# Kernel optimization log

Measured on AMD Instinct MI355X. Metric: run time of the kernel, lower is better.

The kernel has to match this reference:

```python
import jax, jax.numpy as jnp
import numpy as np

N_EMBD = 384
N_HEAD = 6
HEAD_SIZE = N_EMBD // N_HEAD
D_FF = 4 * N_EMBD
LN_EPS = 1e-3  # keras LayerNormalization default epsilon


def setup_inputs() -> dict:
    key = jax.random.key(0)
    ks = jax.random.split(key, 12)
    B, T = 4, 2048
    s = 1.0 / np.sqrt(N_EMBD)
    return {
        "x": jax.random.normal(ks[0], (B, T, N_EMBD), dtype=jnp.float32),
        "Wq": jax.random.normal(ks[1], (N_EMBD, N_EMBD), dtype=jnp.float32) * s,
        "Wk": jax.random.normal(ks[2], (N_EMBD, N_EMBD), dtype=jnp.float32) * s,
        "Wv": jax.random.normal(ks[3], (N_EMBD, N_EMBD), dtype=jnp.float32) * s,
        "Wo": jax.random.normal(ks[4], (N_EMBD, N_EMBD), dtype=jnp.float32) * s,
        "bo": jnp.zeros((N_EMBD,), dtype=jnp.float32),
        "W1": jax.random.normal(ks[5], (N_EMBD, D_FF), dtype=jnp.float32) * s,
        "b1": jnp.zeros((D_FF,), dtype=jnp.float32),
        "W2": jax.random.normal(ks[6], (D_FF, N_EMBD), dtype=jnp.float32) * (1.0 / np.sqrt(D_FF)),
        "b2": jnp.zeros((N_EMBD,), dtype=jnp.float32),
        "g1": jnp.ones((N_EMBD,), dtype=jnp.float32),
        "be1": jnp.zeros((N_EMBD,), dtype=jnp.float32),
        "g2": jnp.ones((N_EMBD,), dtype=jnp.float32),
        "be2": jnp.zeros((N_EMBD,), dtype=jnp.float32),
    }


def _layer_norm(x, gamma, beta):
    mu = jnp.mean(x, axis=-1, keepdims=True)
    var = jnp.mean(jnp.square(x - mu), axis=-1, keepdims=True)
    return (x - mu) * jax.lax.rsqrt(var + LN_EPS) * gamma + beta


def _block(x, Wq, Wk, Wv, Wo, bo, W1, b1, W2, b2, g1, be1, g2, be2):
    B, T, C = x.shape
    H, D = N_HEAD, HEAD_SIZE
    q = (x @ Wq).reshape(B, T, H, D).transpose(0, 2, 1, 3)  # [B,H,T,D]
    k = (x @ Wk).reshape(B, T, H, D).transpose(0, 2, 1, 3)
    v = (x @ Wv).reshape(B, T, H, D).transpose(0, 2, 1, 3)
    scores = jnp.einsum("bhqd,bhkd->bhqk", q, k) / jnp.sqrt(jnp.float32(D))
    causal = jnp.tril(jnp.ones((T, T), dtype=bool))
    scores = jnp.where(causal, scores, jnp.float32(-1e9))
    attn = jax.nn.softmax(scores, axis=-1)  # dropout is identity at inference
    out = jnp.einsum("bhqk,bhkd->bhqd", attn, v)
    out = out.transpose(0, 2, 1, 3).reshape(B, T, H * D)
    y = out @ Wo + bo
    x = _layer_norm(x + y, g1, be1)
    y = jax.nn.relu(x @ W1 + b1) @ W2 + b2
    return _layer_norm(x + y, g2, be2)


def reference(x, Wq, Wk, Wv, Wo, bo, W1, b1, W2, b2, g1, be1, g2, be2):
    return _block(x, Wq, Wk, Wv, Wo, bo, W1, b1, W2, b2, g1, be1, g2, be2)
```

## Files before the change

kernel.cpp:

```cpp
#include <hip/hip_runtime.h>

#define C_DIM  384
#define HEADS  6
#define HD     64
#define FF_DIM 1536
#define LN_EPS 1e-3f
#define TSEQ   2048
#define BATCH  4
#define LOG2E  1.4426950408889634f
#define QK_SCALE 0.18033688011112042f

typedef __attribute__((ext_vector_type(4))) float          f32x4;
typedef __attribute__((ext_vector_type(4))) float          float4_t;
typedef __attribute__((ext_vector_type(8))) short          bfrag;
typedef __attribute__((ext_vector_type(4))) unsigned short ushort4_t;
typedef __attribute__((ext_vector_type(8))) unsigned short ushort8_t;

__device__ inline unsigned short f2bf(float f) {
    unsigned int u = __builtin_bit_cast(unsigned int, f);
    u += 0x7fff + ((u >> 16) & 1);
    return (unsigned short)(u >> 16);
}
__device__ inline unsigned short f2bf_t(float f) {
    return (unsigned short)(__builtin_bit_cast(unsigned int, f) >> 16);
}

__device__ inline void gload_lds16(const void* g, void* l) {
    __builtin_amdgcn_global_load_lds(
        (const __attribute__((address_space(1))) unsigned int*)g,
        (__attribute__((address_space(3))) unsigned int*)l,
        16, 0, 0);
}

__global__ __launch_bounds__(256)
void transpose_w4(const float* __restrict__ Wq, const float* __restrict__ Wk,
                  const float* __restrict__ Wv, const float* __restrict__ Wo,
                  unsigned short* __restrict__ Dq, unsigned short* __restrict__ Dk,
                  unsigned short* __restrict__ Dv, unsigned short* __restrict__ Do_)
{
    __shared__ float tile[32][33];
    const int z = blockIdx.z;
    const float* W = z == 0 ? Wq : (z == 1 ? Wk : (z == 2 ? Wv : Wo));
    unsigned short* D = z == 0 ? Dq : (z == 1 ? Dk : (z == 2 ? Dv : Do_));
    const int tx = threadIdx.x, ty = threadIdx.y;
    const int n0 = blockIdx.x * 32, k0 = blockIdx.y * 32;
    #pragma unroll
    for (int i = 0; i < 32; i += 8)
        tile[ty + i][tx] = W[(size_t)(k0 + ty + i) * C_DIM + n0 + tx];
    __syncthreads();
    #pragma unroll
    for (int i = 0; i < 32; i += 8)
        D[(size_t)(n0 + ty + i) * C_DIM + k0 + tx] = f2bf(tile[tx][ty + i]);
}

__global__ __launch_bounds__(256)
void transpose_w(const float* __restrict__ W, unsigned short* __restrict__ Wt, int K, int N)
{
    __shared__ float tile[32][33];
    const int tx = threadIdx.x, ty = threadIdx.y;
    const int n0 = blockIdx.x * 32, k0 = blockIdx.y * 32;
    #pragma unroll
    for (int i = 0; i < 32; i += 8)
        tile[ty + i][tx] = W[(size_t)(k0 + ty + i) * N + n0 + tx];
    __syncthreads();
    #pragma unroll
    for (int i = 0; i < 32; i += 8)
        Wt[(size_t)(n0 + ty + i) * K + k0 + tx] = f2bf(tile[tx][ty + i]);
}

__global__ __launch_bounds__(256)
void cvt_f32_bf16_x4(const float* __restrict__ in, unsigned short* __restrict__ out, int n4)
{
    int i = blockIdx.x * 256 + threadIdx.x;
    if (i >= n4) return;
    float4_t v = ((const float4_t*)in)[i];
    ushort4_t o = { f2bf(v.x), f2bf(v.y), f2bf(v.z), f2bf(v.w) };
    ((ushort4_t*)out)[i] = o;
}

__global__ __launch_bounds__(256)
void vtrans_kernel(const unsigned short* __restrict__ qkv,
                   unsigned short* __restrict__ vt,
                   unsigned short* __restrict__ ktc)
{
    __shared__ unsigned short tile[32][34];
    const int tx = threadIdx.x, ty = threadIdx.y;
    const int bh = blockIdx.z, b = bh / HEADS, h = bh % HEADS;
    const int t0 = blockIdx.x * 32, d0 = blockIdx.y * 32;
    #pragma unroll
    for (int i = 0; i < 32; i += 8) {
        tile[ty + i][tx] = qkv[(size_t)(b * TSEQ + t0 + ty + i) * 1152 + 2 * C_DIM + h * HD + d0 + tx];
        ktc[((size_t)bh * TSEQ + t0 + ty + i) * HD + d0 + tx] =
            qkv[(size_t)(b * TSEQ + t0 + ty + i) * 1152 + C_DIM + h * HD + d0 + tx];
    }
    __syncthreads();
    #pragma unroll
    for (int i = 0; i < 32; i += 8)
        vt[((size_t)bh * HD + d0 + ty + i) * TSEQ + t0 + tx] = tile[tx][ty + i];
}

template<int OBF16, int BIAS, int RELU, int QSCALE>
__global__ __launch_bounds__(256)
void gemm_lds(const unsigned short* __restrict__ A, const unsigned short* __restrict__ Bt,
              const float* __restrict__ bias, void* __restrict__ Cv,
              int M, int N, int K)
{
    __shared__ __align__(16) unsigned short As[16 * 512];
    __shared__ __align__(16) unsigned short Bs[16 * 512];

    const int t = threadIdx.x, lane = t & 63, w = t >> 6;
    const int ln16 = lane & 15, hi16 = lane >> 4;
    const int wr = w >> 1, wc = w & 1;
    const int row0 = blockIdx.y * 128, col0 = blockIdx.x * 128;

    f32x4 acc[4][4] = {};

    for (int k0 = 0; k0 < K; k0 += 64) {
        #pragma unroll
        for (int i = 0; i < 4; ++i) {
            const int f  = w * 4 + i;
            const int ks = f >> 3, rf = f & 7;
            const int row = rf * 16 + ln16;
            const int kc  = k0 + ks * 32 + hi16 * 8;
            gload_lds16(&A [(size_t)(row0 + row) * K + kc], &As[f * 512]);
            gload_lds16(&Bt[(size_t)(col0 + row) * K + kc], &Bs[f * 512]);
        }
        __syncthreads();
        #pragma unroll
        for (int ks = 0; ks < 2; ++ks) {
            bfrag a[4], b[4];
            #pragma unroll
            for (int i = 0; i < 4; ++i)
                a[i] = *(const bfrag*)&As[(ks * 8 + wr * 4 + i) * 512 + lane * 8];
            #pragma unroll
            for (int j = 0; j < 4; ++j)
                b[j] = *(const bfrag*)&Bs[(ks * 8 + wc * 4 + j) * 512 + lane * 8];
            #pragma unroll
            for (int i = 0; i < 4; ++i)
                #pragma unroll
                for (int j = 0; j < 4; ++j)
                    acc[i][j] = __builtin_amdgcn_mfma_f32_16x16x32_bf16(a[i], b[j], acc[i][j], 0, 0, 0);
        }
        __syncthreads();
    }

    #pragma unroll
    for (int j = 0; j < 4; ++j) {
        const int col = col0 + wc * 64 + j * 16 + ln16;
        const float bv = BIAS ? bias[col] : 0.0f;
        const float sc = (QSCALE && col < C_DIM) ? QK_SCALE : 1.0f;
        #pragma unroll
        for (int i = 0; i < 4; ++i) {
            #pragma unroll
            for (int e = 0; e < 4; ++e) {
                const int row = row0 + wr * 64 + i * 16 + hi16 * 4 + e;
                float v = acc[i][j][e] + bv;
                if (RELU) v = fmaxf(v, 0.0f);
                if (QSCALE) v *= sc;
                if (OBF16) ((unsigned short*)Cv)[(size_t)row * N + col] = f2bf(v);
                else       ((float*)Cv)[(size_t)row * N + col] = v;
            }
        }
    }
}

template<int OBF16, int BIAS, int RELU>
__global__ __launch_bounds__(256)
void gemm_lds64(const unsigned short* __restrict__ A, const unsigned short* __restrict__ Bt,
                const float* __restrict__ bias, void* __restrict__ Cv,
                int M, int N, int K)
{
    __shared__ __align__(16) unsigned short As[8 * 512];
    __shared__ __align__(16) unsigned short Bs[16 * 512];

    const int t = threadIdx.x, lane = t & 63, w = t >> 6;
    const int ln16 = lane & 15, hi16 = lane >> 4;
    const int wr = w >> 1, wc = w & 1;
    const int row0 = blockIdx.y * 64, col0 = blockIdx.x * 128;

    f32x4 acc[2][4] = {};

    for (int k0 = 0; k0 < K; k0 += 64) {
        #pragma unroll
        for (int i = 0; i < 2; ++i) {
            const int f  = w * 2 + i;
            const int ks = f >> 2, rf = f & 3;
            gload_lds16(&A[(size_t)(row0 + rf * 16 + ln16) * K + k0 + ks * 32 + hi16 * 8],
                        &As[f * 512]);
        }
        #pragma unroll
        for (int i = 0; i < 4; ++i) {
            const int f  = w * 4 + i;
            const int ks = f >> 3, cf = f & 7;
            gload_lds16(&Bt[(size_t)(col0 + cf * 16 + ln16) * K + k0 + ks * 32 + hi16 * 8],
                        &Bs[f * 512]);
        }
        __syncthreads();
        #pragma unroll
        for (int ks = 0; ks < 2; ++ks) {
            bfrag a[2], b[4];
            #pragma unroll
            for (int i = 0; i < 2; ++i)
                a[i] = *(const bfrag*)&As[(ks * 4 + wr * 2 + i) * 512 + lane * 8];
            #pragma unroll
            for (int j = 0; j < 4; ++j)
                b[j] = *(const bfrag*)&Bs[(ks * 8 + wc * 4 + j) * 512 + lane * 8];
            #pragma unroll
            for (int i = 0; i < 2; ++i)
                #pragma unroll
                for (int j = 0; j < 4; ++j)
                    acc[i][j] = __builtin_amdgcn_mfma_f32_16x16x32_bf16(a[i], b[j], acc[i][j], 0, 0, 0);
        }
        __syncthreads();
    }

    #pragma unroll
    for (int j = 0; j < 4; ++j) {
        const int col = col0 + wc * 64 + j * 16 + ln16;
        const float bv = BIAS ? bias[col] : 0.0f;
        #pragma unroll
        for (int i = 0; i < 2; ++i) {
            #pragma unroll
            for (int e = 0; e < 4; ++e) {
                const int row = row0 + wr * 32 + i * 16 + hi16 * 4 + e;
                float v = acc[i][j][e] + bv;
                if (RELU) v = fmaxf(v, 0.0f);
                if (OBF16) ((unsigned short*)Cv)[(size_t)row * N + col] = f2bf(v);
                else       ((float*)Cv)[(size_t)row * N + col] = v;
            }
        }
    }
}

__device__ inline void qk16(const bfrag (&qf)[2][2], const bfrag (&kf)[4][2],
                            f32x4 (&sf)[2][4])
{
    #pragma unroll
    for (int jt = 0; jt < 4; ++jt)
        #pragma unroll
        for (int ks = 0; ks < 2; ++ks) {
            sf[0][jt] = __builtin_amdgcn_mfma_f32_16x16x32_bf16(qf[0][ks], kf[jt][ks], sf[0][jt], 0, 0, 0);
            sf[1][jt] = __builtin_amdgcn_mfma_f32_16x16x32_bf16(qf[1][ks], kf[jt][ks], sf[1][jt], 0, 0, 0);
        }
}

__device__ inline void softmax_pv(f32x4 (&sf)[2][4], const bfrag (&vf)[4][2],
                                  f32x4 (&acc)[2][4],
                                  float (&mrow)[2][4], float (&lrow)[2][4],
                                  unsigned short (*Ps)[72],
                                  int tok0, int kt, bool last, int ln16, int hi16)
{
    float lmax[2][4];
    bool need = false;
    #pragma unroll
    for (int rf = 0; rf < 2; ++rf)
        #pragma unroll
        for (int e = 0; e < 4; ++e) {
            const int row = tok0 + rf * 16 + hi16 * 4 + e;
            float mx = -1e30f;
            #pragma unroll
            for (int jt = 0; jt < 4; ++jt) {
                float sv = sf[rf][jt][e];
                if (last && (kt * 64 + jt * 16 + ln16 > row)) sv = -1e30f;
                mx = fmaxf(mx, sv);
            }
            lmax[rf][e] = mx;
            need = need || (mx > mrow[rf][e] + 8.0f);
        }
    if (__any(need)) {
        #pragma unroll
        for (int rf = 0; rf < 2; ++rf)
            #pragma unroll
            for (int e = 0; e < 4; ++e) {
                float rm = lmax[rf][e];
                rm = fmaxf(rm, __shfl_xor(rm, 1));
                rm = fmaxf(rm, __shfl_xor(rm, 2));
                rm = fmaxf(rm, __shfl_xor(rm, 4));
                rm = fmaxf(rm, __shfl_xor(rm, 8));
                const float mn = fmaxf(mrow[rf][e], rm);
                const float corr = exp2f(mrow[rf][e] - mn);
                mrow[rf][e] = mn;
                lrow[rf][e] *= corr;
                #pragma unroll
                for (int dt = 0; dt < 4; ++dt) acc[rf][dt][e] *= corr;
            }
    }

    #pragma unroll
    for (int rf = 0; rf < 2; ++rf)
        #pragma unroll
        for (int jt = 0; jt < 4; ++jt)
            #pragma unroll
            for (int e = 0; e < 4; ++e) {
                const int row = tok0 + rf * 16 + hi16 * 4 + e;
                float sv = sf[rf][jt][e];
                if (last && (kt * 64 + jt * 16 + ln16 > row)) sv = -1e30f;
                const float pe = exp2f(sv - mrow[rf][e]);
                lrow[rf][e] += pe;
                Ps[rf * 16 + hi16 * 4 + e][jt * 16 + ln16] = f2bf_t(pe);
            }

    bfrag pf[2][2];
    #pragma unroll
    for (int rf = 0; rf < 2; ++rf)
        #pragma unroll
        for (int ks = 0; ks < 2; ++ks)
            pf[rf][ks] = *(const bfrag*)&Ps[rf * 16 + ln16][ks * 32 + hi16 * 8];
    #pragma unroll
    for (int ks = 0; ks < 2; ++ks)
        #pragma unroll
        for (int rf = 0; rf < 2; ++rf)
            #pragma unroll
            for (int dt = 0; dt < 4; ++dt)
                acc[rf][dt] = __builtin_amdgcn_mfma_f32_16x16x32_bf16(pf[rf][ks], vf[dt][ks], acc[rf][dt], 0, 0, 0);
}

__global__ __launch_bounds__(64)
void attn_kernel(const unsigned short* __restrict__ qkv,
                 const unsigned short* __restrict__ ktc,
                 const unsigned short* __restrict__ vt,
                 unsigned short* __restrict__ att,
                 unsigned short* __restrict__ pacc,
                 float* __restrict__ pml)
{
    __shared__ __align__(16) unsigned short Ps[32][72];
    const int lane = threadIdx.x;
    const int ln16 = lane & 15, hi16 = lane >> 4;
    const int bid = blockIdx.x;
    const int xcd = bid & 7;
    const int i   = bid >> 3;
    int bh, qw, kt0, kte, ck = 0;
    bool heavy;
    if (i < 192) {
        qw = 63 - (i / 6);
        const int r = i % 6;
        bh = xcd * 3 + (r >> 1);
        ck = r & 1;
        const int NT = (qw >> 1) + 1;
        const int half = NT >> 1;
        kt0 = ck ? half : 0;
        kte = ck ? NT : half;
        heavy = true;
    } else {
        const int j = i - 192;
        qw = 31 - (j / 3);
        bh = xcd * 3 + (j % 3);
        kt0 = 0;
        kte = (qw >> 1) + 1;
        heavy = false;
    }
    const int NTfull = (qw >> 1) + 1;
    const int b = bh / HEADS, h = bh % HEADS;
    const int tok0 = qw * 32;
    const size_t qrow0 = (size_t)b * TSEQ;

    bfrag qf[2][2];
    #pragma unroll
    for (int rf = 0; rf < 2; ++rf)
        #pragma unroll
        for (int ks = 0; ks < 2; ++ks)
            qf[rf][ks] = *(const bfrag*)&qkv[(qrow0 + tok0 + rf * 16 + ln16) * 1152 + h * HD + ks * 32 + hi16 * 8];

    f32x4 acc[2][4] = {};
    float mrow[2][4], lrow[2][4];
    #pragma unroll
    for (int rf = 0; rf < 2; ++rf)
        #pragma unroll
        for (int e = 0; e < 4; ++e) { mrow[rf][e] = -1e30f; lrow[rf][e] = 0.0f; }

    const unsigned short* Kb = ktc + (size_t)bh * TSEQ * HD;
    const unsigned short* Vb = vt  + (size_t)bh * HD * TSEQ;

    bfrag kf[4][2];
    #pragma unroll
    for (int jt = 0; jt < 4; ++jt)
        #pragma unroll
        for (int ks = 0; ks < 2; ++ks)
            kf[jt][ks] = *(const bfrag*)&Kb[(size_t)(kt0 * 64 + jt * 16 + ln16) * HD + ks * 32 + hi16 * 8];

    for (int kt = kt0; kt < kte; ++kt) {
        bfrag vf[4][2];
        #pragma unroll
        for (int dt = 0; dt < 4; ++dt)
            #pragma unroll
            for (int ks = 0; ks < 2; ++ks)
                vf[dt][ks] = *(const bfrag*)&Vb[(size_t)(dt * 16 + ln16) * TSEQ + kt * 64 + ks * 32 + hi16 * 8];

        f32x4 sf[2][4] = {};
        qk16(qf, kf, sf);

        if (kt + 1 < kte) {
            #pragma unroll
            for (int jt = 0; jt < 4; ++jt)
                #pragma unroll
                for (int ks = 0; ks < 2; ++ks)
                    kf[jt][ks] = *(const bfrag*)&Kb[(size_t)((kt + 1) * 64 + jt * 16 + ln16) * HD + ks * 32 + hi16 * 8];
        }

        softmax_pv(sf, vf, acc, mrow, lrow, Ps, tok0, kt, kt == NTfull - 1, ln16, hi16);
    }

    float lsum[2][4];
    #pragma unroll
    for (int rf = 0; rf < 2; ++rf)
        #pragma unroll
        for (int e = 0; e < 4; ++e) {
            float l = lrow[rf][e];
            l += __shfl_xor(l, 1);
            l += __shfl_xor(l, 2);
            l += __shfl_xor(l, 4);
            l += __shfl_xor(l, 8);
            lsum[rf][e] = l;
        }

    if (!heavy) {
        #pragma unroll
        for (int rf = 0; rf < 2; ++rf)
            #pragma unroll
            for (int e = 0; e < 4; ++e) {
                const float inv = 1.0f / lsum[rf][e];
                const size_t row = qrow0 + tok0 + rf * 16 + hi16 * 4 + e;
                #pragma unroll
                for (int dt = 0; dt < 4; ++dt)
                    att[row * C_DIM + h * HD + dt * 16 + ln16] = f2bf(acc[rf][dt][e] * inv);
            }
    } else {
        const int sidx = bh * 32 + (qw - 32);
        const size_t pb = (size_t)sidx * 2 + ck;
        #pragma unroll
        for (int rf = 0; rf < 2; ++rf)
            #pragma unroll
            for (int dt = 0; dt < 4; ++dt)
                #pragma unroll
                for (int e = 0; e < 4; ++e) {
                    const int row = rf * 16 + hi16 * 4 + e;
                    pacc[(pb * 32 + row) * 64 + dt * 16 + ln16] = f2bf(acc[rf][dt][e]);
                }
        if (ln16 == 0) {
            #pragma unroll
            for (int rf = 0; rf < 2; ++rf)
                #pragma unroll
                for (int e = 0; e < 4; ++e) {
                    const int row = rf * 16 + hi16 * 4 + e;
                    pml[pb * 64 + row * 2 + 0] = mrow[rf][e];
                    pml[pb * 64 + row * 2 + 1] = lsum[rf][e];
                }
        }
    }
}

__global__ __launch_bounds__(256)
void attn_combine(const unsigned short* __restrict__ pacc,
                  const float* __restrict__ pml,
                  unsigned short* __restrict__ att)
{
    const int sidx = blockIdx.x;
    const int bh = sidx >> 5;
    const int qw = 32 + (sidx & 31);
    const int b = bh / HEADS, h = bh % HEADS;
    const int tid = threadIdx.x;
    const int row = tid >> 3;
    const int d0  = (tid & 7) * 8;

    const float m0 = pml[((size_t)sidx * 2 + 0) * 64 + row * 2 + 0];
    const float l0 = pml[((size_t)sidx * 2 + 0) * 64 + row * 2 + 1];
    const float m1 = pml[((size_t)sidx * 2 + 1) * 64 + row * 2 + 0];
    const float l1 = pml[((size_t)sidx * 2 + 1) * 64 + row * 2 + 1];
    const float M  = fmaxf(m0, m1);
    const float w0 = exp2f(m0 - M), w1 = exp2f(m1 - M);
    const float invL = 1.0f / (l0 * w0 + l1 * w1);

    ushort8_t a0 = *(const ushort8_t*)&pacc[(((size_t)sidx * 2 + 0) * 32 + row) * 64 + d0];
    ushort8_t a1 = *(const ushort8_t*)&pacc[(((size_t)sidx * 2 + 1) * 32 + row) * 64 + d0];
    ushort8_t rv;
    #pragma unroll
    for (int k = 0; k < 8; ++k) {
        const float v0 = __builtin_bit_cast(float, (unsigned int)a0[k] << 16);
        const float v1 = __builtin_bit_cast(float, (unsigned int)a1[k] << 16);
        rv[k] = f2bf((v0 * w0 + v1 * w1) * invL);
    }
    const size_t grow = (size_t)b * TSEQ + qw * 32 + row;
    *(ushort8_t*)&att[grow * C_DIM + h * HD + d0] = rv;
}

template<int WB>
__global__ __launch_bounds__(256)
void ln_residual_kernel(const float* __restrict__ A, const float* __restrict__ R,
                        const float* __restrict__ gamma, const float* __restrict__ beta,
                        float* __restrict__ out, unsigned short* __restrict__ outb, int Mrows)
{
    const int lane = threadIdx.x & 63;
    const int wv   = threadIdx.x >> 6;
    const int row  = blockIdx.x * 4 + wv;
    if (row >= Mrows) return;
    const size_t off = (size_t)row * C_DIM;

    float v[6];
    float sum = 0.0f;
    #pragma unroll
    for (int j = 0; j < 6; ++j) {
        const int c = lane + 64 * j;
        v[j] = A[off + c] + R[off + c];
        sum += v[j];
    }
    #pragma unroll
    for (int o = 1; o < 64; o <<= 1) sum += __shfl_xor(sum, o);
    const float mu = sum * (1.0f / C_DIM);

    float sq = 0.0f;
    #pragma unroll
    for (int j = 0; j < 6; ++j) { const float d = v[j] - mu; sq = fmaf(d, d, sq); }
    #pragma unroll
    for (int o = 1; o < 64; o <<= 1) sq += __shfl_xor(sq, o);
    const float rstd = rsqrtf(sq * (1.0f / C_DIM) + LN_EPS);

    #pragma unroll
    for (int j = 0; j < 6; ++j) {
        const int c = lane + 64 * j;
        const float r = (v[j] - mu) * rstd * gamma[c] + beta[c];
        out[off + c] = r;
        if (WB) outb[off + c] = f2bf(r);
    }
}

extern "C" void kernel_launch(void* const* d_in, const int* in_sizes, int n_in,
                              void* d_out, int out_size, void* d_ws, size_t ws_size,
                              hipStream_t stream)
{
    const float* x   = (const float*)d_in[0];
    const float* Wq  = (const float*)d_in[1];
    const float* Wk  = (const float*)d_in[2];
    const float* Wv  = (const float*)d_in[3];
    const float* Wo  = (const float*)d_in[4];
    const float* bo  = (const float*)d_in[5];
    const float* W1  = (const float*)d_in[6];
    const float* b1  = (const float*)d_in[7];
    const float* W2  = (const float*)d_in[8];
    const float* b2  = (const float*)d_in[9];
    const float* g1  = (const float*)d_in[10];
    const float* be1 = (const float*)d_in[11];
    const float* g2  = (const float*)d_in[12];
    const float* be2 = (const float*)d_in[13];
    float* out = (float*)d_out;

    const int M = BATCH * TSEQ;
    const size_t MC = (size_t)M * C_DIM;

    char* ws = (char*)d_ws;
    unsigned short* qkv = (unsigned short*)ws;
    unsigned short* vt  = (unsigned short*)(ws + (size_t)M*1152*2);
    unsigned short* att = (unsigned short*)(ws + (size_t)M*1152*2 + (size_t)BATCH*HEADS*HD*TSEQ*2);
    unsigned short* h1  = (unsigned short*)ws;
    char* p2 = ws + (size_t)M*1152*2 + (size_t)BATCH*HEADS*HD*TSEQ*2 + MC*2;
    unsigned short* xb  = (unsigned short*)p2;
    unsigned short* ktc = xb;
    float* y   = (float*)(p2 + MC*2);
    float* x1  = (float*)(p2 + MC*2 + MC*4);
    unsigned short* x1b = (unsigned short*)(p2 + MC*2 + 2*MC*4);
    char* p3 = p2 + MC*2 + 2*MC*4 + MC*2;
    unsigned short* Wqkv_t = (unsigned short*)p3;
    unsigned short* Wo_t   = Wqkv_t + (size_t)3*C_DIM*C_DIM;
    unsigned short* W1_t   = Wo_t   + (size_t)C_DIM*C_DIM;
    unsigned short* W2_t   = W1_t   + (size_t)FF_DIM*C_DIM;

    unsigned short* pacc = (unsigned short*)(p2 + MC*2);
    float* pml = (float*)(p2 + MC*2 + (size_t)1536*32*64*2);

    dim3 b256(256), b328(32, 8);

    transpose_w4<<<dim3(C_DIM/32, C_DIM/32, 4), b328, 0, stream>>>(
        Wq, Wk, Wv, Wo,
        Wqkv_t, Wqkv_t + (size_t)C_DIM*C_DIM, Wqkv_t + (size_t)2*C_DIM*C_DIM, Wo_t);
    transpose_w<<<dim3(FF_DIM/32, C_DIM/32), b328, 0, stream>>>(W1, W1_t, C_DIM, FF_DIM);
    transpose_w<<<dim3(C_DIM/32, FF_DIM/32), b328, 0, stream>>>(W2, W2_t, FF_DIM, C_DIM);

    cvt_f32_bf16_x4<<<dim3((MC/4 + 255)/256), b256, 0, stream>>>(x, xb, (int)(MC/4));

    gemm_lds<1, 0, 0, 1><<<dim3(3*C_DIM/128, M/128), b256, 0, stream>>>(
        xb, Wqkv_t, nullptr, qkv, M, 3*C_DIM, C_DIM);

    vtrans_kernel<<<dim3(TSEQ/32, HD/32, BATCH*HEADS), b328, 0, stream>>>(qkv, vt, ktc);

    attn_kernel<<<dim3(2304), dim3(64), 0, stream>>>(qkv, ktc, vt, att, pacc, pml);
    attn_combine<<<dim3(768), b256, 0, stream>>>(pacc, pml, att);

    gemm_lds64<0, 1, 0><<<dim3(C_DIM/128, M/64), b256, 0, stream>>>(
        att, Wo_t, bo, y, M, C_DIM, C_DIM);

    ln_residual_kernel<1><<<dim3(M/4), b256, 0, stream>>>(x, y, g1, be1, x1, x1b, M);

    gemm_lds<1, 1, 1, 0><<<dim3(FF_DIM/128, M/128), b256, 0, stream>>>(
        x1b, W1_t, b1, h1, M, FF_DIM, C_DIM);

    gemm_lds64<0, 1, 0><<<dim3(C_DIM/128, M/64), b256, 0, stream>>>(
        h1, W2_t, b2, y, M, C_DIM, FF_DIM);

    ln_residual_kernel<0><<<dim3(M/4), b256, 0, stream>>>(x1, y, g2, be2, out, nullptr, M);
}
```

Baseline: 204.1 us.

## Merge weight transposes, fuse K relayout into QKV GEMM, drop fp32 x1

Combines the three weight transpose kernels into one launch. Moves the K-head relayout into the QKV GEMM epilogue so vtrans only transposes V. Adds s_setprio around the MFMA blocks in attention. Removes the fp32 copy of the post-LN1 activations and feeds the bf16 copy into the final residual LayerNorm, which cuts memory traffic but lowers residual precision.

```diff
diff --git a/kernel.cpp b/kernel.cpp
--- a/kernel.cpp
+++ b/kernel.cpp
@@ -24,6 +24,9 @@
 __device__ inline unsigned short f2bf_t(float f) {
     return (unsigned short)(__builtin_bit_cast(unsigned int, f) >> 16);
 }
+__device__ inline float bf2f(unsigned short u) {
+    return __builtin_bit_cast(float, (unsigned int)u << 16);
+}
 
 __device__ inline void gload_lds16(const void* g, void* l) {
     __builtin_amdgcn_global_load_lds(
@@ -33,39 +36,37 @@
 }
 
 __global__ __launch_bounds__(256)
-void transpose_w4(const float* __restrict__ Wq, const float* __restrict__ Wk,
-                  const float* __restrict__ Wv, const float* __restrict__ Wo,
-                  unsigned short* __restrict__ Dq, unsigned short* __restrict__ Dk,
-                  unsigned short* __restrict__ Dv, unsigned short* __restrict__ Do_)
+void transpose_all(const float* __restrict__ Wq, const float* __restrict__ Wk,
+                   const float* __restrict__ Wv, const float* __restrict__ Wo,
+                   const float* __restrict__ W1, const float* __restrict__ W2,
+                   unsigned short* __restrict__ Dqkv, unsigned short* __restrict__ Do_,
+                   unsigned short* __restrict__ D1, unsigned short* __restrict__ D2)
 {
     __shared__ float tile[32][33];
-    const int z = blockIdx.z;
-    const float* W = z == 0 ? Wq : (z == 1 ? Wk : (z == 2 ? Wv : Wo));
-    unsigned short* D = z == 0 ? Dq : (z == 1 ? Dk : (z == 2 ? Dv : Do_));
+    const int bidx = blockIdx.x;
+    const float* W; unsigned short* D;
+    int K, N, nx, ny;
+    if (bidx < 576) {
+        const int z = bidx / 144, r = bidx % 144;
+        W = z == 0 ? Wq : (z == 1 ? Wk : (z == 2 ? Wv : Wo));
+        D = z == 3 ? Do_ : Dqkv + (size_t)z * C_DIM * C_DIM;
+        K = N = C_DIM; nx = r % 12; ny = r / 12;
+    } else if (bidx < 1152) {
+        const int r = bidx - 576;
+        W = W1; D = D1; K = C_DIM; N = FF_DIM; nx = r % 48; ny = r / 48;
+    } else {
+        const int r = bidx - 1152;
+        W = W2; D = D2; K = FF_DIM; N = C_DIM; nx = r % 12; ny = r / 12;
+    }
     const int tx = threadIdx.x, ty = threadIdx.y;
-    const int n0 = blockIdx.x * 32, k0 = blockIdx.y * 32;
-    #pragma unroll
-    for (int i = 0; i < 32; i += 8)
-        tile[ty + i][tx] = W[(size_t)(k0 + ty + i) * C_DIM + n0 + tx];
-    __syncthreads();
-    #pragma unroll
-    for (int i = 0; i < 32; i += 8)
-        D[(size_t)(n0 + ty + i) * C_DIM + k0 + tx] = f2bf(tile[tx][ty + i]);
-}
-
-__global__ __launch_bounds__(256)
-void transpose_w(const float* __restrict__ W, unsigned short* __restrict__ Wt, int K, int N)
-{
-    __shared__ float tile[32][33];
-    const int tx = threadIdx.x, ty = threadIdx.y;
-    const int n0 = blockIdx.x * 32, k0 = blockIdx.y * 32;
+    const int n0 = nx * 32, k0 = ny * 32;
     #pragma unroll
     for (int i = 0; i < 32; i += 8)
         tile[ty + i][tx] = W[(size_t)(k0 + ty + i) * N + n0 + tx];
     __syncthreads();
     #pragma unroll
     for (int i = 0; i < 32; i += 8)
-        Wt[(size_t)(n0 + ty + i) * K + k0 + tx] = f2bf(tile[tx][ty + i]);
+        D[(size_t)(n0 + ty + i) * K + k0 + tx] = f2bf(tile[tx][ty + i]);
 }
 
 __global__ __launch_bounds__(256)
@@ -80,29 +81,26 @@
 
 __global__ __launch_bounds__(256)
 void vtrans_kernel(const unsigned short* __restrict__ qkv,
-                   unsigned short* __restrict__ vt,
-                   unsigned short* __restrict__ ktc)
+                   unsigned short* __restrict__ vt)
 {
     __shared__ unsigned short tile[32][34];
     const int tx = threadIdx.x, ty = threadIdx.y;
     const int bh = blockIdx.z, b = bh / HEADS, h = bh % HEADS;
     const int t0 = blockIdx.x * 32, d0 = blockIdx.y * 32;
     #pragma unroll
-    for (int i = 0; i < 32; i += 8) {
+    for (int i = 0; i < 32; i += 8)
         tile[ty + i][tx] = qkv[(size_t)(b * TSEQ + t0 + ty + i) * 1152 + 2 * C_DIM + h * HD + d0 + tx];
-        ktc[((size_t)bh * TSEQ + t0 + ty + i) * HD + d0 + tx] =
-            qkv[(size_t)(b * TSEQ + t0 + ty + i) * 1152 + C_DIM + h * HD + d0 + tx];
-    }
     __syncthreads();
     #pragma unroll
     for (int i = 0; i < 32; i += 8)
         vt[((size_t)bh * HD + d0 + ty + i) * TSEQ + t0 + tx] = tile[tx][ty + i];
 }
 
-template<int OBF16, int BIAS, int RELU, int QSCALE>
+template<int OBF16, int BIAS, int RELU, int QSCALE, int KSPLIT>
 __global__ __launch_bounds__(256)
 void gemm_lds(const unsigned short* __restrict__ A, const unsigned short* __restrict__ Bt,
               const float* __restrict__ bias, void* __restrict__ Cv,
+              unsigned short* __restrict__ ktc,
               int M, int N, int K)
 {
     __shared__ __align__(16) unsigned short As[16 * 512];
@@ -146,9 +144,11 @@
 
     #pragma unroll
     for (int j = 0; j < 4; ++j) {
-        const int col = col0 + wc * 64 + j * 16 + ln16;
+        const int cbase = col0 + wc * 64 + j * 16;
+        const int col = cbase + ln16;
         const float bv = BIAS ? bias[col] : 0.0f;
         const float sc = (QSCALE && col < C_DIM) ? QK_SCALE : 1.0f;
+        const bool kdest = KSPLIT && (cbase >= C_DIM) && (cbase < 2 * C_DIM);
         #pragma unroll
         for (int i = 0; i < 4; ++i) {
             #pragma unroll
@@ -157,8 +157,16 @@
                 float v = acc[i][j][e] + bv;
                 if (RELU) v = fmaxf(v, 0.0f);
                 if (QSCALE) v *= sc;
-                if (OBF16) ((unsigned short*)Cv)[(size_t)row * N + col] = f2bf(v);
-                else       ((float*)Cv)[(size_t)row * N + col] = v;
+                if (kdest) {
+                    const int b  = row >> 11, tt = row & 2047;
+                    const int hd = col - C_DIM;
+                    const int bh = b * HEADS + (hd >> 6);
+                    ktc[((size_t)bh * TSEQ + tt) * HD + (hd & 63)] = f2bf(v);
+                } else if (OBF16) {
+                    ((unsigned short*)Cv)[(size_t)row * N + col] = f2bf(v);
+                } else {
+                    ((float*)Cv)[(size_t)row * N + col] = v;
+                }
             }
         }
     }
@@ -235,6 +243,7 @@
 __device__ inline void qk16(const bfrag (&qf)[2][2], const bfrag (&kf)[4][2],
                             f32x4 (&sf)[2][4])
 {
+    __builtin_amdgcn_s_setprio(1);
     #pragma unroll
     for (int jt = 0; jt < 4; ++jt)
         #pragma unroll
@@ -242,6 +251,7 @@
             sf[0][jt] = __builtin_amdgcn_mfma_f32_16x16x32_bf16(qf[0][ks], kf[jt][ks], sf[0][jt], 0, 0, 0);
             sf[1][jt] = __builtin_amdgcn_mfma_f32_16x16x32_bf16(qf[1][ks], kf[jt][ks], sf[1][jt], 0, 0, 0);
         }
+    __builtin_amdgcn_s_setprio(0);
 }
 
 __device__ inline void softmax_pv(f32x4 (&sf)[2][4], const bfrag (&vf)[4][2],
@@ -306,6 +316,7 @@
         #pragma unroll
         for (int ks = 0; ks < 2; ++ks)
             pf[rf][ks] = *(const bfrag*)&Ps[rf * 16 + ln16][ks * 32 + hi16 * 8];
+    __builtin_amdgcn_s_setprio(1);
     #pragma unroll
     for (int ks = 0; ks < 2; ++ks)
         #pragma unroll
@@ -313,6 +324,7 @@
             #pragma unroll
             for (int dt = 0; dt < 4; ++dt)
                 acc[rf][dt] = __builtin_amdgcn_mfma_f32_16x16x32_bf16(pf[rf][ks], vf[dt][ks], acc[rf][dt], 0, 0, 0);
+    __builtin_amdgcn_s_setprio(0);
 }
 
 __global__ __launch_bounds__(64)
@@ -475,17 +487,17 @@
     ushort8_t rv;
     #pragma unroll
     for (int k = 0; k < 8; ++k) {
-        const float v0 = __builtin_bit_cast(float, (unsigned int)a0[k] << 16);
-        const float v1 = __builtin_bit_cast(float, (unsigned int)a1[k] << 16);
+        const float v0 = bf2f(a0[k]);
+        const float v1 = bf2f(a1[k]);
         rv[k] = f2bf((v0 * w0 + v1 * w1) * invL);
     }
     const size_t grow = (size_t)b * TSEQ + qw * 32 + row;
     *(ushort8_t*)&att[grow * C_DIM + h * HD + d0] = rv;
 }
 
-template<int WB>
+template<int ABF16, int WF32, int WBF>
 __global__ __launch_bounds__(256)
-void ln_residual_kernel(const float* __restrict__ A, const float* __restrict__ R,
+void ln_residual_kernel(const void* __restrict__ Av, const float* __restrict__ R,
                         const float* __restrict__ gamma, const float* __restrict__ beta,
                         float* __restrict__ out, unsigned short* __restrict__ outb, int Mrows)
 {
@@ -500,7 +512,9 @@
     #pragma unroll
     for (int j = 0; j < 6; ++j) {
         const int c = lane + 64 * j;
-        v[j] = A[off + c] + R[off + c];
+        const float a = ABF16 ? bf2f(((const unsigned short*)Av)[off + c])
+                              : ((const float*)Av)[off + c];
+        v[j] = a + R[off + c];
         sum += v[j];
     }
     #pragma unroll
@@ -518,8 +532,8 @@
     for (int j = 0; j < 6; ++j) {
         const int c = lane + 64 * j;
         const float r = (v[j] - mu) * rstd * gamma[c] + beta[c];
-        out[off + c] = r;
-        if (WB) outb[off + c] = f2bf(r);
+        if (WF32) out[off + c] = r;
+        if (WBF)  outb[off + c] = f2bf(r);
     }
 }
 
@@ -553,9 +567,8 @@
     unsigned short* h1  = (unsigned short*)ws;
     char* p2 = ws + (size_t)M*1152*2 + (size_t)BATCH*HEADS*HD*TSEQ*2 + MC*2;
     unsigned short* xb  = (unsigned short*)p2;
-    unsigned short* ktc = xb;
     float* y   = (float*)(p2 + MC*2);
-    float* x1  = (float*)(p2 + MC*2 + MC*4);
+    unsigned short* ktc = (unsigned short*)(p2 + MC*2 + MC*4);
     unsigned short* x1b = (unsigned short*)(p2 + MC*2 + 2*MC*4);
     char* p3 = p2 + MC*2 + 2*MC*4 + MC*2;
     unsigned short* Wqkv_t = (unsigned short*)p3;
@@ -568,18 +581,15 @@
 
     dim3 b256(256), b328(32, 8);
 
-    transpose_w4<<<dim3(C_DIM/32, C_DIM/32, 4), b328, 0, stream>>>(
-        Wq, Wk, Wv, Wo,
-        Wqkv_t, Wqkv_t + (size_t)C_DIM*C_DIM, Wqkv_t + (size_t)2*C_DIM*C_DIM, Wo_t);
-    transpose_w<<<dim3(FF_DIM/32, C_DIM/32), b328, 0, stream>>>(W1, W1_t, C_DIM, FF_DIM);
-    transpose_w<<<dim3(C_DIM/32, FF_DIM/32), b328, 0, stream>>>(W2, W2_t, FF_DIM, C_DIM);
+    transpose_all<<<dim3(1728), b328, 0, stream>>>(
+        Wq, Wk, Wv, Wo, W1, W2, Wqkv_t, Wo_t, W1_t, W2_t);
 
     cvt_f32_bf16_x4<<<dim3((MC/4 + 255)/256), b256, 0, stream>>>(x, xb, (int)(MC/4));
 
-    gemm_lds<1, 0, 0, 1><<<dim3(3*C_DIM/128, M/128), b256, 0, stream>>>(
-        xb, Wqkv_t, nullptr, qkv, M, 3*C_DIM, C_DIM);
-
-    vtrans_kernel<<<dim3(TSEQ/32, HD/32, BATCH*HEADS), b328, 0, stream>>>(qkv, vt, ktc);
+    gemm_lds<1, 0, 0, 1, 1><<<dim3(3*C_DIM/128, M/128), b256, 0, stream>>>(
+        xb, Wqkv_t, nullptr, qkv, ktc, M, 3*C_DIM, C_DIM);
+
+    vtrans_kernel<<<dim3(TSEQ/32, HD/32, BATCH*HEADS), b328, 0, stream>>>(qkv, vt);
 
     attn_kernel<<<dim3(2304), dim3(64), 0, stream>>>(qkv, ktc, vt, att, pacc, pml);
     attn_combine<<<dim3(768), b256, 0, stream>>>(pacc, pml, att);
@@ -587,13 +597,15 @@
     gemm_lds64<0, 1, 0><<<dim3(C_DIM/128, M/64), b256, 0, stream>>>(
         att, Wo_t, bo, y, M, C_DIM, C_DIM);
 
-    ln_residual_kernel<1><<<dim3(M/4), b256, 0, stream>>>(x, y, g1, be1, x1, x1b, M);
-
-    gemm_lds<1, 1, 1, 0><<<dim3(FF_DIM/128, M/128), b256, 0, stream>>>(
-        x1b, W1_t, b1, h1, M, FF_DIM, C_DIM);
+    ln_residual_kernel<0, 0, 1><<<dim3(M/4), b256, 0, stream>>>(
+        x, y, g1, be1, nullptr, x1b, M);
+
+    gemm_lds<1, 1, 1, 0, 0><<<dim3(FF_DIM/128, M/128), b256, 0, stream>>>(
+        x1b, W1_t, b1, h1, nullptr, M, FF_DIM, C_DIM);
 
     gemm_lds64<0, 1, 0><<<dim3(C_DIM/128, M/64), b256, 0, stream>>>(
         h1, W2_t, b2, y, M, C_DIM, FF_DIM);
 
-    ln_residual_kernel<0><<<dim3(M/4), b256, 0, stream>>>(x1, y, g2, be2, out, nullptr, M);
-}
+    ln_residual_kernel<1, 1, 0><<<dim3(M/4), b256, 0, stream>>>(
+        x1b, y, g2, be2, out, nullptr, M);
+}
```

After: 195.4 us. 4.3% less time.
